# Optimization experiments

Hardware: AMD Instinct MI355X
Metric: run time of the kernel (lower is better)

## Reference

```python
import jax, jax.numpy as jnp
import numpy as np

K = 2                 # top-k experts per token
CAP_FACTOR = 1.25     # capacity factor


def setup_inputs() -> dict:
    key = jax.random.key(0)
    ks = jax.random.split(key, 6)
    B, T, C, H, E = 8, 2048, 1024, 4096, 8
    return {
        "x":  jax.random.normal(ks[0], (B, T, C), dtype=jnp.float32),
        "Wr": jax.random.normal(ks[1], (C, E), dtype=jnp.float32) * 0.02,
        "W1": jax.random.normal(ks[2], (E, C, H), dtype=jnp.float32) * 0.02,
        "b1": jax.random.normal(ks[3], (E, H), dtype=jnp.float32) * 0.02,
        "W2": jax.random.normal(ks[4], (E, H, C), dtype=jnp.float32) * 0.02,
        "b2": jax.random.normal(ks[5], (E, C), dtype=jnp.float32) * 0.02,
    }


def reference(x, Wr, W1, b1, W2, b2):
    B, T, C = x.shape
    E = Wr.shape[1]
    capacity = int(T / E * CAP_FACTOR)  # per (expert, batch-row) bucket, as in torch code

    # Router: probs over experts, top-k selection
    probs = jax.nn.softmax(x @ Wr, axis=-1)                  # [B,T,E]
    topk_probs, topk_experts = jax.lax.top_k(probs, K)       # [B,T,K]

    # Flatten token slots in (t, k) order -- matches torch nonzero() enumeration
    S = T * K
    e_flat = topk_experts.reshape(B, S)                      # [B,S] int32
    p_flat = topk_probs.reshape(B, S)                        # [B,S]
    x_rep = jnp.repeat(x, K, axis=1)                         # [B,S,C]; slot (t,k) -> x[b,t]

    # Position of each slot within its (batch-row b, expert e) group
    onehot = jax.nn.one_hot(e_flat, E, dtype=jnp.int32)      # [B,S,E]
    pos_all = jnp.cumsum(onehot, axis=1) - onehot            # position before self
    pos = jnp.take_along_axis(pos_all, e_flat[..., None], axis=-1)[..., 0]  # [B,S]
    keep = pos < capacity                                    # tokens beyond capacity dropped
    pos_c = jnp.minimum(pos, capacity - 1)

    # Dispatch: scatter kept tokens into [E, B, capacity, C] buffer (padding_val = 0)
    b_idx = jnp.broadcast_to(jnp.arange(B)[:, None], (B, S))
    buf = jnp.zeros((E, B, capacity, C), dtype=x.dtype)
    buf = buf.at[e_flat, b_idx, pos_c].add(x_rep * keep[..., None].astype(x.dtype))

    # Expert FFN (grouped GEMM): Linear -> ReLU -> Linear, one weight set per expert
    h = jax.nn.relu(jnp.einsum('ebnc,ech->ebnh', buf, W1) + b1[:, None, None, :])
    y = jnp.einsum('ebnh,ehc->ebnc', h, W2) + b2[:, None, None, :]

    # Combine: gather back, zero dropped slots, weight by router prob, sum over k
    y_tok = y[e_flat, b_idx, pos_c]                          # [B,S,C]
    y_tok = y_tok * (keep[..., None].astype(x.dtype)) * p_flat[..., None]
    out = y_tok.reshape(B, T, K, C).sum(axis=2)              # [B,T,C]
    return out
```

## Files before the change

kernel.cpp:

```cpp
#include <hip/hip_runtime.h>

#define B_ 8
#define T_ 2048
#define C_ 1024
#define H_ 4096
#define E_ 8
#define S_ (2 * T_)
#define CAP 320
#define ME 2560
#define NROWS (E_ * ME)

typedef __attribute__((ext_vector_type(8))) short short8;
typedef __attribute__((ext_vector_type(4))) float f32x4;

__device__ __forceinline__ unsigned short f2bf(float f) {
  unsigned u = __float_as_uint(f);
  unsigned r = 0x7FFFu + ((u >> 16) & 1u);
  return (unsigned short)((u + r) >> 16);
}
__device__ __forceinline__ float bf2f(unsigned short u) {
  return __uint_as_float(((unsigned)u) << 16);
}

__device__ __forceinline__ void gload_lds16(const void* g, void* l) {
  __builtin_amdgcn_global_load_lds(
      (const __attribute__((address_space(1))) unsigned int*)g,
      (__attribute__((address_space(3))) unsigned int*)l, 16, 0, 0);
}

__global__ void cvt_transpose(const float* __restrict__ in,
                              unsigned short* __restrict__ out, int R, int Cc) {
  __shared__ float t[64][65];
  const int tid = threadIdx.x;
  const long eoff = (long)blockIdx.z * R * Cc;
  const int r0 = blockIdx.x * 64, c0 = blockIdx.y * 64;
#pragma unroll
  for (int it = 0; it < 4; ++it) {
    int r = it * 16 + (tid >> 4);
    int c = (tid & 15) * 4;
    float4 v = *(const float4*)(in + eoff + (long)(r0 + r) * Cc + c0 + c);
    t[r][c] = v.x; t[r][c + 1] = v.y; t[r][c + 2] = v.z; t[r][c + 3] = v.w;
  }
  __syncthreads();
#pragma unroll
  for (int it = 0; it < 4; ++it) {
    int oc = it * 16 + (tid >> 4);
    int orr = (tid & 15) * 4;
    union { unsigned short u[4]; unsigned long long ll; } o;
    o.u[0] = f2bf(t[orr + 0][oc]); o.u[1] = f2bf(t[orr + 1][oc]);
    o.u[2] = f2bf(t[orr + 2][oc]); o.u[3] = f2bf(t[orr + 3][oc]);
    *(unsigned long long*)(out + eoff + (long)(c0 + oc) * R + r0 + orr) = o.ll;
  }
}

__global__ void router_cvt(const float* __restrict__ x, const float* __restrict__ Wr,
                           int* __restrict__ es, float* __restrict__ ps,
                           unsigned short* __restrict__ x_bf) {
  const int token = blockIdx.x * 4 + (threadIdx.x >> 6);
  const int lane = threadIdx.x & 63;
  const float* xr = x + (long)token * C_;
  float acc[8] = {0, 0, 0, 0, 0, 0, 0, 0};
#pragma unroll
  for (int j = 0; j < 4; ++j) {
    int c = j * 256 + lane * 4;
    float4 xv = *(const float4*)(xr + c);
    union { unsigned short u[4]; unsigned long long ll; } o;
    o.u[0] = f2bf(xv.x); o.u[1] = f2bf(xv.y); o.u[2] = f2bf(xv.z); o.u[3] = f2bf(xv.w);
    *(unsigned long long*)(x_bf + (long)token * C_ + c) = o.ll;
    const float xe[4] = {xv.x, xv.y, xv.z, xv.w};
#pragma unroll
    for (int i = 0; i < 4; ++i) {
      const float4* wr = (const float4*)(Wr + (long)(c + i) * 8);
      float4 w0 = wr[0], w1 = wr[1];
      float v = xe[i];
      acc[0] += v * w0.x; acc[1] += v * w0.y; acc[2] += v * w0.z; acc[3] += v * w0.w;
      acc[4] += v * w1.x; acc[5] += v * w1.y; acc[6] += v * w1.z; acc[7] += v * w1.w;
    }
  }
#pragma unroll
  for (int off = 32; off >= 1; off >>= 1)
#pragma unroll
    for (int e = 0; e < 8; ++e) acc[e] += __shfl_xor(acc[e], off);
  float mx = acc[0];
#pragma unroll
  for (int e = 1; e < 8; ++e) mx = fmaxf(mx, acc[e]);
  float pr[8], se = 0.f;
#pragma unroll
  for (int e = 0; e < 8; ++e) { pr[e] = expf(acc[e] - mx); se += pr[e]; }
  float inv = 1.f / se;
  int e0 = 0; float v0 = pr[0];
#pragma unroll
  for (int e = 1; e < 8; ++e) if (pr[e] > v0) { v0 = pr[e]; e0 = e; }
  int e1 = -1; float v1 = -1.f;
#pragma unroll
  for (int e = 0; e < 8; ++e) if (e != e0 && pr[e] > v1) { v1 = pr[e]; e1 = e; }
  if (lane == 0) {
    es[2 * token] = e0;     ps[2 * token] = v0 * inv;
    es[2 * token + 1] = e1; ps[2 * token + 1] = v1 * inv;
  }
}

__global__ void positions(const int* __restrict__ es, int* __restrict__ pos,
                          int* __restrict__ tsrc) {
  const int b = blockIdx.x;
  const int lane = threadIdx.x;
  int cnt[8] = {0, 0, 0, 0, 0, 0, 0, 0};
  unsigned long long below = (1ULL << lane) - 1ULL;
  int e_next = es[(long)b * S_ + lane];
  for (int chunk = 0; chunk < S_ / 64; ++chunk) {
    int e = e_next;
    if (chunk + 1 < S_ / 64) e_next = es[(long)b * S_ + (chunk + 1) * 64 + lane];
    int myPos = 0;
#pragma unroll
    for (int ei = 0; ei < 8; ++ei) {
      unsigned long long m = __ballot(e == ei);
      if (e == ei) myPos = cnt[ei] + __popcll(m & below);
      cnt[ei] += __popcll(m);
    }
    int s = chunk * 64 + lane;
    pos[(long)b * S_ + s] = myPos;
    if (myPos < CAP)
      tsrc[(long)e * ME + b * CAP + myPos] = b * T_ + (s >> 1);
  }
}

template <bool GATHER, bool RELU>
__global__ __launch_bounds__(512, 2) void moe_gemm256(
    const unsigned short* __restrict__ A, const unsigned short* __restrict__ BT,
    const float* __restrict__ bias, const int* __restrict__ tsrc,
    unsigned short* __restrict__ outp, const int Kfull, const int Kslice,
    const int NT, const int KS) {
  constexpr int BK = 64;
  constexpr int MT = ME / 256;
  __shared__ unsigned short As[2][2][256 * 32];
  __shared__ unsigned short Bs[2][2][256 * 32];
  const int tid = threadIdx.x, lane = tid & 63, w = tid >> 6;
  const int wr = w >> 2, wc = w & 3;
  const int N = NT * 256;

  const int nwg = E_ * KS * NT * MT;
  const int chunk = nwg >> 3;
  const int swz = (blockIdx.x & 7) * chunk + (blockIdx.x >> 3);
  const int mt = swz % MT;
  int rem = swz / MT;
  const int nt = rem % NT; rem /= NT;
  const int ks = rem % KS;
  const int e = rem / KS;
  const int n0 = nt * 256;
  const long ksoff = (long)ks * Kslice;

  const int srow = lane >> 2;
  const int psrc = ((lane & 3) ^ ((lane >> 3) & 3)) << 3;
  const unsigned short* aSrc[2];
  const unsigned short* bSrc[2];
#pragma unroll
  for (int i = 0; i < 2; ++i) {
    int r = i * 128 + w * 16 + srow;
    long rowbase;
    if constexpr (GATHER) {
      int xrow = tsrc[(long)e * ME + mt * 256 + r];
      if (xrow < 0) xrow = 0;
      rowbase = (long)xrow * Kfull;
    } else {
      rowbase = ((long)e * ME + mt * 256 + r) * (long)Kfull;
    }
    aSrc[i] = A + rowbase + ksoff + psrc;
    bSrc[i] = BT + ((long)e * N + n0 + i * 128 + w * 16 + srow) * (long)Kfull +
              ksoff + psrc;
  }

  f32x4 acc[8][4];
#pragma unroll
  for (int m = 0; m < 8; ++m)
#pragma unroll
    for (int n = 0; n < 4; ++n) acc[m][n] = (f32x4){0.f, 0.f, 0.f, 0.f};

  const int l15 = lane & 15, l4 = lane >> 4;
  const int rslot = ((l4 ^ ((l15 >> 1) & 3)) << 3);

#pragma unroll
  for (int s = 0; s < 2; ++s) {
#pragma unroll
    for (int i = 0; i < 2; ++i)
      gload_lds16(aSrc[i] + s * 32, &As[0][s][(i * 128 + w * 16) * 32]);
#pragma unroll
    for (int i = 0; i < 2; ++i)
      gload_lds16(bSrc[i] + s * 32, &Bs[0][s][(i * 128 + w * 16) * 32]);
  }
  asm volatile("s_waitcnt vmcnt(4)" ::: "memory");
  __builtin_amdgcn_s_barrier();
  __builtin_amdgcn_sched_barrier(0);

  const int nkt = Kslice / BK;
  for (int kt = 0; kt < nkt; ++kt) {
    const int cur = kt & 1, nxt = cur ^ 1;
    const bool pf = (kt + 1 < nkt);
    const long koff = (long)(kt + 1) * BK;
#pragma unroll
    for (int s = 0; s < 2; ++s) {
      short8 bf[4], af[8];
#pragma unroll
      for (int n = 0; n < 4; ++n) {
        int rb = wc * 64 + n * 16 + l15;
        bf[n] = *(const short8*)&Bs[cur][s][rb * 32 + rslot];
      }
#pragma unroll
      for (int m = 0; m < 8; ++m) {
        int r = wr * 128 + m * 16 + l15;
        af[m] = *(const short8*)&As[cur][s][r * 32 + rslot];
      }
      if (pf) {
#pragma unroll
        for (int i = 0; i < 2; ++i)
          gload_lds16(aSrc[i] + koff + s * 32, &As[nxt][s][(i * 128 + w * 16) * 32]);
#pragma unroll
        for (int i = 0; i < 2; ++i)
          gload_lds16(bSrc[i] + koff + s * 32, &Bs[nxt][s][(i * 128 + w * 16) * 32]);
      }
      __builtin_amdgcn_s_setprio(1);
#pragma unroll
      for (int m = 0; m < 8; ++m)
#pragma unroll
        for (int n = 0; n < 4; ++n)
          acc[m][n] = __builtin_amdgcn_mfma_f32_16x16x32_bf16(af[m], bf[n],
                                                              acc[m][n], 0, 0, 0);
      __builtin_amdgcn_s_setprio(0);
      __builtin_amdgcn_sched_barrier(0);
      if (s == 0) {
        if (pf) asm volatile("s_waitcnt vmcnt(4)" ::: "memory");
        else    asm volatile("s_waitcnt vmcnt(0)" ::: "memory");
        __builtin_amdgcn_s_barrier();
      } else if (pf) {
        asm volatile("s_waitcnt vmcnt(4)" ::: "memory");
        __builtin_amdgcn_s_barrier();
      }
      __builtin_amdgcn_sched_barrier(0);
    }
  }
  __builtin_amdgcn_sched_barrier(0);

  const long rbase = (long)ks * NROWS + (long)e * ME + mt * 256;
#pragma unroll
  for (int m = 0; m < 8; ++m) {
#pragma unroll
    for (int n = 0; n < 4; ++n) {
      const int trow = wr * 128 + m * 16 + (l4 << 2);
      const int col = n0 + wc * 64 + n * 16 + l15;
      const float bv = (ks == 0) ? bias[(long)e * N + col] : 0.f;
#pragma unroll
      for (int j = 0; j < 4; ++j) {
        float v = acc[m][n][j] + bv;
        if constexpr (RELU) v = fmaxf(v, 0.f);
        outp[(rbase + trow + j) * (long)N + col] = f2bf(v);
      }
    }
  }
}

__global__ void combine(const unsigned short* __restrict__ y,
                        const int* __restrict__ es, const float* __restrict__ ps,
                        const int* __restrict__ pos, float* __restrict__ out) {
  const int token = blockIdx.x;
  const int b = token >> 11;
  const int s0 = 2 * token, s1 = s0 + 1;
  int e0 = es[s0], e1 = es[s1];
  int q0 = pos[s0], q1 = pos[s1];
  float p0 = ps[s0], p1 = ps[s1];
  const bool k0 = q0 < CAP, k1 = q1 < CAP;
  if (q0 > CAP - 1) q0 = CAP - 1;
  if (q1 > CAP - 1) q1 = CAP - 1;
  const long half = (long)NROWS * C_;
  const unsigned short* r0 = y + ((long)e0 * ME + b * CAP + q0) * C_;
  const unsigned short* r1 = y + ((long)e1 * ME + b * CAP + q1) * C_;
  const int c = threadIdx.x * 4;
  float4 a = {0.f, 0.f, 0.f, 0.f};
  if (k0) {
    union { unsigned short u[4]; unsigned long long ll; } v, vv;
    v.ll = *(const unsigned long long*)(r0 + c);
    vv.ll = *(const unsigned long long*)(r0 + half + c);
    a.x += p0 * (bf2f(v.u[0]) + bf2f(vv.u[0]));
    a.y += p0 * (bf2f(v.u[1]) + bf2f(vv.u[1]));
    a.z += p0 * (bf2f(v.u[2]) + bf2f(vv.u[2]));
    a.w += p0 * (bf2f(v.u[3]) + bf2f(vv.u[3]));
  }
  if (k1) {
    union { unsigned short u[4]; unsigned long long ll; } v, vv;
    v.ll = *(const unsigned long long*)(r1 + c);
    vv.ll = *(const unsigned long long*)(r1 + half + c);
    a.x += p1 * (bf2f(v.u[0]) + bf2f(vv.u[0]));
    a.y += p1 * (bf2f(v.u[1]) + bf2f(vv.u[1]));
    a.z += p1 * (bf2f(v.u[2]) + bf2f(vv.u[2]));
    a.w += p1 * (bf2f(v.u[3]) + bf2f(vv.u[3]));
  }
  *(float4*)(out + (long)token * C_ + c) = a;
}

extern "C" void kernel_launch(void* const* d_in, const int* in_sizes, int n_in,
                              void* d_out, int out_size, void* d_ws, size_t ws_size,
                              hipStream_t stream) {
  const float* x = (const float*)d_in[0];
  const float* Wr = (const float*)d_in[1];
  const float* W1 = (const float*)d_in[2];
  const float* b1 = (const float*)d_in[3];
  const float* W2 = (const float*)d_in[4];
  const float* b2 = (const float*)d_in[5];
  float* out = (float*)d_out;
  char* ws = (char*)d_ws;
  unsigned short* x_bf = (unsigned short*)(ws + 0L);
  unsigned short* W1T = (unsigned short*)(ws + 33554432L);
  unsigned short* W2T = (unsigned short*)(ws + 100663296L);
  unsigned short* h = (unsigned short*)(ws + 167772160L);
  unsigned short* y = (unsigned short*)(ws + 335544320L);
  int* es = (int*)(ws + 419430400L);
  float* ps = (float*)(ws + 419561472L);
  int* pos = (int*)(ws + 419692544L);
  int* tsrc = (int*)(ws + 419823616L);

  cvt_transpose<<<dim3(16, 64, 8), 256, 0, stream>>>(W1, W1T, C_, H_);
  cvt_transpose<<<dim3(64, 16, 8), 256, 0, stream>>>(W2, W2T, H_, C_);
  router_cvt<<<4096, 256, 0, stream>>>(x, Wr, es, ps, x_bf);
  hipMemsetAsync(tsrc, 0xFF, NROWS * sizeof(int), stream);
  positions<<<8, 64, 0, stream>>>(es, pos, tsrc);
  moe_gemm256<true, true><<<1280, 512, 0, stream>>>(x_bf, W1T, b1, tsrc, h,
                                                    C_, C_, 16, 1);
  moe_gemm256<false, false><<<640, 512, 0, stream>>>(h, W2T, b2, nullptr, y,
                                                     H_, H_ / 2, 4, 2);
  combine<<<16384, 256, 0, stream>>>(y, es, ps, pos, out);
}
```

Baseline: 596.8 us.

## Use 4-stage LDS ring pipeline and split-K=4 for second expert GEMM

The GEMM main loop moves from a double-buffered 64-wide K step to a four-slot ring of 32-wide K segments with three segments in flight, aiming to hide more global-load latency. The second GEMM's K dimension is split four ways instead of two, doubling the workgroup count to 1280 for better CU occupancy. Partial outputs are written to two buffers, one reusing the x_bf region, and combine sums four bf16 partials. This adds partial-output traffic and extra rounding from an additional bf16 partial, and Kslice is now hardcoded to 1024.

```diff
diff --git a/kernel.cpp b/kernel.cpp
--- a/kernel.cpp
+++ b/kernel.cpp
@@ -128,12 +128,12 @@
 __global__ __launch_bounds__(512, 2) void moe_gemm256(
     const unsigned short* __restrict__ A, const unsigned short* __restrict__ BT,
     const float* __restrict__ bias, const int* __restrict__ tsrc,
-    unsigned short* __restrict__ outp, const int Kfull, const int Kslice,
-    const int NT, const int KS) {
-  constexpr int BK = 64;
+    unsigned short* __restrict__ out01, unsigned short* __restrict__ out23,
+    const int Kfull, const int NT, const int KS) {
   constexpr int MT = ME / 256;
-  __shared__ unsigned short As[2][2][256 * 32];
-  __shared__ unsigned short Bs[2][2][256 * 32];
+  constexpr int SEG = 32;
+  __shared__ unsigned short As[4][256 * 32];
+  __shared__ unsigned short Bs[4][256 * 32];
   const int tid = threadIdx.x, lane = tid & 63, w = tid >> 6;
   const int wr = w >> 2, wc = w & 3;
   const int N = NT * 256;
@@ -147,7 +147,7 @@
   const int ks = rem % KS;
   const int e = rem / KS;
   const int n0 = nt * 256;
-  const long ksoff = (long)ks * Kslice;
+  const long ksoff = (long)ks * 1024;
 
   const int srow = lane >> 2;
   const int psrc = ((lane & 3) ^ ((lane >> 3) & 3)) << 3;
@@ -179,67 +179,70 @@
   const int rslot = ((l4 ^ ((l15 >> 1) & 3)) << 3);
 
 #pragma unroll
-  for (int s = 0; s < 2; ++s) {
+  for (int s = 0; s < 3; ++s) {
 #pragma unroll
     for (int i = 0; i < 2; ++i)
-      gload_lds16(aSrc[i] + s * 32, &As[0][s][(i * 128 + w * 16) * 32]);
+      gload_lds16(aSrc[i] + s * 32, &As[s][(i * 128 + w * 16) * 32]);
 #pragma unroll
     for (int i = 0; i < 2; ++i)
-      gload_lds16(bSrc[i] + s * 32, &Bs[0][s][(i * 128 + w * 16) * 32]);
-  }
+      gload_lds16(bSrc[i] + s * 32, &Bs[s][(i * 128 + w * 16) * 32]);
+  }
+  asm volatile("s_waitcnt vmcnt(8)" ::: "memory");
+  __builtin_amdgcn_s_barrier();
+  __builtin_amdgcn_sched_barrier(0);
+
+  auto seg = [&](int t, bool doStage) {
+    const int cb = t & 3;
+    short8 bf[4], af[8];
+#pragma unroll
+    for (int n = 0; n < 4; ++n) {
+      int rb = wc * 64 + n * 16 + l15;
+      bf[n] = *(const short8*)&Bs[cb][rb * 32 + rslot];
+    }
+#pragma unroll
+    for (int m = 0; m < 8; ++m) {
+      int r = wr * 128 + m * 16 + l15;
+      af[m] = *(const short8*)&As[cb][r * 32 + rslot];
+    }
+    if (doStage) {
+      const int nb = (t + 3) & 3;
+      const long koff = (long)(t + 3) * 32;
+#pragma unroll
+      for (int i = 0; i < 2; ++i)
+        gload_lds16(aSrc[i] + koff, &As[nb][(i * 128 + w * 16) * 32]);
+#pragma unroll
+      for (int i = 0; i < 2; ++i)
+        gload_lds16(bSrc[i] + koff, &Bs[nb][(i * 128 + w * 16) * 32]);
+    }
+    __builtin_amdgcn_s_setprio(1);
+#pragma unroll
+    for (int m = 0; m < 8; ++m)
+#pragma unroll
+      for (int n = 0; n < 4; ++n)
+        acc[m][n] = __builtin_amdgcn_mfma_f32_16x16x32_bf16(af[m], bf[n],
+                                                            acc[m][n], 0, 0, 0);
+    __builtin_amdgcn_s_setprio(0);
+    __builtin_amdgcn_sched_barrier(0);
+  };
+
+  for (int t = 0; t < SEG - 3; ++t) {
+    seg(t, true);
+    asm volatile("s_waitcnt vmcnt(8)" ::: "memory");
+    __builtin_amdgcn_s_barrier();
+    __builtin_amdgcn_sched_barrier(0);
+  }
+  seg(SEG - 3, false);
   asm volatile("s_waitcnt vmcnt(4)" ::: "memory");
   __builtin_amdgcn_s_barrier();
   __builtin_amdgcn_sched_barrier(0);
-
-  const int nkt = Kslice / BK;
-  for (int kt = 0; kt < nkt; ++kt) {
-    const int cur = kt & 1, nxt = cur ^ 1;
-    const bool pf = (kt + 1 < nkt);
-    const long koff = (long)(kt + 1) * BK;
-#pragma unroll
-    for (int s = 0; s < 2; ++s) {
-      short8 bf[4], af[8];
-#pragma unroll
-      for (int n = 0; n < 4; ++n) {
-        int rb = wc * 64 + n * 16 + l15;
-        bf[n] = *(const short8*)&Bs[cur][s][rb * 32 + rslot];
-      }
-#pragma unroll
-      for (int m = 0; m < 8; ++m) {
-        int r = wr * 128 + m * 16 + l15;
-        af[m] = *(const short8*)&As[cur][s][r * 32 + rslot];
-      }
-      if (pf) {
-#pragma unroll
-        for (int i = 0; i < 2; ++i)
-          gload_lds16(aSrc[i] + koff + s * 32, &As[nxt][s][(i * 128 + w * 16) * 32]);
-#pragma unroll
-        for (int i = 0; i < 2; ++i)
-          gload_lds16(bSrc[i] + koff + s * 32, &Bs[nxt][s][(i * 128 + w * 16) * 32]);
-      }
-      __builtin_amdgcn_s_setprio(1);
-#pragma unroll
-      for (int m = 0; m < 8; ++m)
-#pragma unroll
-        for (int n = 0; n < 4; ++n)
-          acc[m][n] = __builtin_amdgcn_mfma_f32_16x16x32_bf16(af[m], bf[n],
-                                                              acc[m][n], 0, 0, 0);
-      __builtin_amdgcn_s_setprio(0);
-      __builtin_amdgcn_sched_barrier(0);
-      if (s == 0) {
-        if (pf) asm volatile("s_waitcnt vmcnt(4)" ::: "memory");
-        else    asm volatile("s_waitcnt vmcnt(0)" ::: "memory");
-        __builtin_amdgcn_s_barrier();
-      } else if (pf) {
-        asm volatile("s_waitcnt vmcnt(4)" ::: "memory");
-        __builtin_amdgcn_s_barrier();
-      }
-      __builtin_amdgcn_sched_barrier(0);
-    }
-  }
+  seg(SEG - 2, false);
+  asm volatile("s_waitcnt vmcnt(0)" ::: "memory");
+  __builtin_amdgcn_s_barrier();
   __builtin_amdgcn_sched_barrier(0);
-
-  const long rbase = (long)ks * NROWS + (long)e * ME + mt * 256;
+  seg(SEG - 1, false);
+
+  unsigned short* outp = (ks & 2) ? out23 : out01;
+  const long rbase = (long)(ks & 1) * NROWS + (long)e * ME + mt * 256;
 #pragma unroll
   for (int m = 0; m < 8; ++m) {
 #pragma unroll
@@ -257,7 +260,8 @@
   }
 }
 
-__global__ void combine(const unsigned short* __restrict__ y,
+__global__ void combine(const unsigned short* __restrict__ y01,
+                        const unsigned short* __restrict__ y23,
                         const int* __restrict__ es, const float* __restrict__ ps,
                         const int* __restrict__ pos, float* __restrict__ out) {
   const int token = blockIdx.x;
@@ -270,27 +274,34 @@
   if (q0 > CAP - 1) q0 = CAP - 1;
   if (q1 > CAP - 1) q1 = CAP - 1;
   const long half = (long)NROWS * C_;
-  const unsigned short* r0 = y + ((long)e0 * ME + b * CAP + q0) * C_;
-  const unsigned short* r1 = y + ((long)e1 * ME + b * CAP + q1) * C_;
+  const long o0 = ((long)e0 * ME + b * CAP + q0) * C_;
+  const long o1 = ((long)e1 * ME + b * CAP + q1) * C_;
   const int c = threadIdx.x * 4;
   float4 a = {0.f, 0.f, 0.f, 0.f};
+  union U { unsigned short u[4]; unsigned long long ll; };
   if (k0) {
-    union { unsigned short u[4]; unsigned long long ll; } v, vv;
-    v.ll = *(const unsigned long long*)(r0 + c);
-    vv.ll = *(const unsigned long long*)(r0 + half + c);
-    a.x += p0 * (bf2f(v.u[0]) + bf2f(vv.u[0]));
-    a.y += p0 * (bf2f(v.u[1]) + bf2f(vv.u[1]));
-    a.z += p0 * (bf2f(v.u[2]) + bf2f(vv.u[2]));
-    a.w += p0 * (bf2f(v.u[3]) + bf2f(vv.u[3]));
+    U v0_, v1_, v2_, v3_;
+    v0_.ll = *(const unsigned long long*)(y01 + o0 + c);
+    v1_.ll = *(const unsigned long long*)(y01 + o0 + half + c);
+    v2_.ll = *(const unsigned long long*)(y23 + o0 + c);
+    v3_.ll = *(const unsigned long long*)(y23 + o0 + half + c);
+#pragma unroll
+    for (int i = 0; i < 4; ++i) {
+      float s = bf2f(v0_.u[i]) + bf2f(v1_.u[i]) + bf2f(v2_.u[i]) + bf2f(v3_.u[i]);
+      (&a.x)[i] += p0 * s;
+    }
   }
   if (k1) {
-    union { unsigned short u[4]; unsigned long long ll; } v, vv;
-    v.ll = *(const unsigned long long*)(r1 + c);
-    vv.ll = *(const unsigned long long*)(r1 + half + c);
-    a.x += p1 * (bf2f(v.u[0]) + bf2f(vv.u[0]));
-    a.y += p1 * (bf2f(v.u[1]) + bf2f(vv.u[1]));
-    a.z += p1 * (bf2f(v.u[2]) + bf2f(vv.u[2]));
-    a.w += p1 * (bf2f(v.u[3]) + bf2f(vv.u[3]));
+    U v0_, v1_, v2_, v3_;
+    v0_.ll = *(const unsigned long long*)(y01 + o1 + c);
+    v1_.ll = *(const unsigned long long*)(y01 + o1 + half + c);
+    v2_.ll = *(const unsigned long long*)(y23 + o1 + c);
+    v3_.ll = *(const unsigned long long*)(y23 + o1 + half + c);
+#pragma unroll
+    for (int i = 0; i < 4; ++i) {
+      float s = bf2f(v0_.u[i]) + bf2f(v1_.u[i]) + bf2f(v2_.u[i]) + bf2f(v3_.u[i]);
+      (&a.x)[i] += p1 * s;
+    }
   }
   *(float4*)(out + (long)token * C_ + c) = a;
 }
@@ -310,7 +321,8 @@
   unsigned short* W1T = (unsigned short*)(ws + 33554432L);
   unsigned short* W2T = (unsigned short*)(ws + 100663296L);
   unsigned short* h = (unsigned short*)(ws + 167772160L);
-  unsigned short* y = (unsigned short*)(ws + 335544320L);
+  unsigned short* y01 = (unsigned short*)(ws + 335544320L);
+  unsigned short* y23 = (unsigned short*)(ws + 0L);
   int* es = (int*)(ws + 419430400L);
   float* ps = (float*)(ws + 419561472L);
   int* pos = (int*)(ws + 419692544L);
@@ -321,9 +333,9 @@
   router_cvt<<<4096, 256, 0, stream>>>(x, Wr, es, ps, x_bf);
   hipMemsetAsync(tsrc, 0xFF, NROWS * sizeof(int), stream);
   positions<<<8, 64, 0, stream>>>(es, pos, tsrc);
-  moe_gemm256<true, true><<<1280, 512, 0, stream>>>(x_bf, W1T, b1, tsrc, h,
-                                                    C_, C_, 16, 1);
-  moe_gemm256<false, false><<<640, 512, 0, stream>>>(h, W2T, b2, nullptr, y,
-                                                     H_, H_ / 2, 4, 2);
-  combine<<<16384, 256, 0, stream>>>(y, es, ps, pos, out);
-}
+  moe_gemm256<true, true><<<1280, 512, 0, stream>>>(x_bf, W1T, b1, tsrc, h, h,
+                                                    C_, 16, 1);
+  moe_gemm256<false, false><<<1280, 512, 0, stream>>>(h, W2T, b2, nullptr, y01,
+                                                      y23, H_, 4, 4);
+  combine<<<16384, 256, 0, stream>>>(y01, y23, es, ps, pos, out);
+}
```

Result: slower. 617.1 us (+3.4%).
